# Performance work log

Measured on AMD Instinct MI355X. Metric: run time of the kernel, lower is better.

The kernel has to match this reference:

```python
import jax, jax.numpy as jnp
import numpy as np

# Grid / point-count constants (K-Radar-style sparse voxel grid)
B, Z, Y, X = 4, 40, 1024, 1024
Nr, Nl = 262144, 1048576
W_OCC, W_OFF, W_FEAT = 0.2, 1.0, 1.0
BIG = jnp.int32(1_000_000_000)  # sentinel for unmatched candidates


def _hash_zyx(b, z, y, x):
    # max value B*Z*Y*X ~ 1.7e8, fits int32
    return ((b * Z + z) * Y + y) * X + x


def _make_offsets(R):
    rng = np.arange(-R, R + 1)
    dz, dy, dx = np.meshgrid(rng, rng, rng, indexing='ij')
    return jnp.asarray(np.stack([dz.ravel(), dy.ravel(), dx.ravel()], axis=1), dtype=jnp.int32)  # [K,3]


def setup_inputs() -> dict:
    key = jax.random.key(0)
    k = jax.random.split(key, 10)
    radar_indices = jnp.stack([
        jax.random.randint(k[0], (Nr,), 0, B, dtype=jnp.int32),
        jax.random.randint(k[1], (Nr,), 0, Z, dtype=jnp.int32),
        jax.random.randint(k[2], (Nr,), 0, Y, dtype=jnp.int32),
        jax.random.randint(k[3], (Nr,), 0, X, dtype=jnp.int32)], axis=1)
    lidar_indices = jnp.stack([
        jax.random.randint(k[4], (Nl,), 0, B, dtype=jnp.int32),
        jax.random.randint(k[5], (Nl,), 0, Z, dtype=jnp.int32),
        jax.random.randint(k[6], (Nl,), 0, Y, dtype=jnp.int32),
        jax.random.randint(k[7], (Nl,), 0, X, dtype=jnp.int32)], axis=1)
    pred_feat = jax.random.normal(k[8], (Nr, 4), dtype=jnp.float32)
    pred_occ = jax.random.normal(k[9], (Nr, 1, 1), dtype=jnp.float32)
    lidar_features = jax.random.normal(jax.random.fold_in(key, 77), (Nl, 4), dtype=jnp.float32)
    return {"pred_feat": pred_feat, "pred_occ": pred_occ, "radar_indices": radar_indices,
            "lidar_features": lidar_features, "lidar_indices": lidar_indices, "R": 1}


def _local_match(radar_indices, lidar_indices, lidar_features, R):
    # Build sorted hash table of lidar voxels
    hL = _hash_zyx(lidar_indices[:, 0], lidar_indices[:, 1], lidar_indices[:, 2], lidar_indices[:, 3])
    ordL = jnp.argsort(hL)
    hL_sorted = hL[ordL]

    offs = _make_offsets(R)                      # [K,3]
    K = offs.shape[0]
    b, z, y, x = radar_indices[:, 0], radar_indices[:, 1], radar_indices[:, 2], radar_indices[:, 3]
    zz = jnp.clip(z[:, None] + offs[None, :, 0], 0, Z - 1)   # [Nr,K]
    yy = jnp.clip(y[:, None] + offs[None, :, 1], 0, Y - 1)
    xx = jnp.clip(x[:, None] + offs[None, :, 2], 0, X - 1)
    cand = _hash_zyx(b[:, None], zz, yy, xx).reshape(-1)      # [Nr*K]

    pos = jnp.searchsorted(hL_sorted, cand)                   # [Nr*K]
    safe_pos = jnp.clip(pos, 0, hL_sorted.shape[0] - 1)
    is_member = (pos < hL_sorted.shape[0]) & (hL_sorted[safe_pos] == cand)
    hit = is_member.reshape(-1, K)                            # [Nr,K]

    dL1 = jnp.sum(jnp.abs(offs), axis=1)                      # [K]
    dL1_masked = jnp.where(hit, dL1[None, :], BIG)            # [Nr,K]
    best_k = jnp.argmin(dL1_masked, axis=1)                   # [Nr]
    best = jnp.take_along_axis(dL1_masked, best_k[:, None], axis=1)[:, 0]
    matched = best < BIG                                      # [Nr] bool

    pos_flat = jnp.take_along_axis(pos.reshape(-1, K), best_k[:, None], axis=1)[:, 0]
    lidar_row = ordL[jnp.clip(pos_flat, 0, hL_sorted.shape[0] - 1)]
    gt_feat = jnp.where(matched[:, None], lidar_features[lidar_row], 0.0)  # [Nr, C_lidar]

    sel_z = jnp.take_along_axis(zz, best_k[:, None], axis=1)[:, 0]
    sel_y = jnp.take_along_axis(yy, best_k[:, None], axis=1)[:, 0]
    sel_x = jnp.take_along_axis(xx, best_k[:, None], axis=1)[:, 0]
    gt_offsets = jnp.stack([sel_z - z, sel_y - y, sel_x - x], axis=1).astype(jnp.float32)
    return matched, gt_offsets, gt_feat


def reference(pred_feat, pred_occ, radar_indices, lidar_features, lidar_indices, R):
    matched, gt_d, gt_f = _local_match(radar_indices, lidar_indices, lidar_features, R)
    gt_d = gt_d[:, ::-1]                              # torch.flip(gt_d, dims=[1])
    m = matched.astype(pred_feat.dtype)

    # BCEWithLogitsLoss(mean): logaddexp(0,x) - x*y
    occ_logits = jnp.mean(jnp.squeeze(pred_occ, axis=1), axis=-1)  # [Nr]
    occ_loss = jnp.mean(jnp.logaddexp(0.0, occ_logits) - occ_logits * m)

    cnt = jnp.sum(m)
    # smooth_l1 (beta=1, mean) over matched rows of pred offsets [M,3]
    diff = pred_feat[:, :3] - gt_d
    ad = jnp.abs(diff)
    sl1 = jnp.where(ad < 1.0, 0.5 * diff * diff, ad - 0.5)
    off_loss = jnp.sum(sl1 * m[:, None]) / jnp.maximum(cnt * 3.0, 1.0)
    # l1 (mean) over matched intensity column [M,1]
    feat_loss = jnp.sum(jnp.abs(pred_feat[:, 3:4] - gt_f[:, 3:4]) * m[:, None]) / jnp.maximum(cnt, 1.0)

    return W_OCC * occ_loss + W_OFF * off_loss + W_FEAT * feat_loss
```

## Files before the change

### kernel.cpp

```cpp
#include <hip/hip_runtime.h>
#include <math.h>
#include <limits.h>

#define BD 4
#define ZD 40
#define YD 1024
#define XD 1024
#define BZYX (167772160)

constexpr int BLOCK = 256;
constexpr unsigned SMALL_LOG = 19;
constexpr unsigned long long EMPTY64 = ~0ull;

typedef unsigned uvec4 __attribute__((ext_vector_type(4)));

__device__ __forceinline__ unsigned hash_mix(unsigned x) {
    x ^= x >> 16; x *= 0x7feb352dU;
    x ^= x >> 15; x *= 0x846ca68bU;
    x ^= x >> 16;
    return x;
}

__device__ __forceinline__ float smooth_l1(float d) {
    float ad = fabsf(d);
    return (ad < 1.0f) ? 0.5f * d * d : ad - 0.5f;
}

__device__ __forceinline__ float logaddexp0(float logit) {
    return (logit > 0.0f) ? (logit + log1pf(expf(-logit))) : log1pf(expf(logit));
}

__global__ void clear_bitmap(uvec4* __restrict__ bmv, int bmW4) {
    const uvec4 z = (uvec4)(0u);
    const int stride = gridDim.x * blockDim.x;
    for (int k = blockIdx.x * blockDim.x + threadIdx.x; k < bmW4; k += stride)
        bmv[k] = z;
}


__global__ void build_bitmap(const int4* __restrict__ li, int Nl,
                             unsigned* __restrict__ bm,
                             unsigned* __restrict__ cells,
                             uvec4* __restrict__ stv, int stW4) {
    const int gid = blockIdx.x * blockDim.x + threadIdx.x;
    if (gid < Nl) {
        int4 v = li[gid];
        unsigned cell = ((unsigned)(v.x * ZD + v.y) * YD + v.z) * XD + v.w;
        cells[gid] = cell;
        atomicOr(&bm[cell >> 5], 1u << (cell & 31));
    }
    const uvec4 f = (uvec4)(~0u);
    const int stride = gridDim.x * blockDim.x;
    for (int k = gid; k < stW4; k += stride)
        stv[k] = f;
}

__global__ void __launch_bounds__(BLOCK)
main_match(const float4* __restrict__ pf, const float* __restrict__ occ,
           const int4* __restrict__ ri, const unsigned* __restrict__ bm,
           unsigned long long* __restrict__ stab, unsigned smask,
           const int* __restrict__ Rptr, int Nr,
           int* __restrict__ mcell, double* __restrict__ partials) {
    const int R = *Rptr;
    const int i = blockIdx.x * BLOCK + threadIdx.x;
    double occ_s = 0.0, cnt_s = 0.0, off_s = 0.0;

    if (i < Nr) {
        int4 rib = ri[i];
        const int b = rib.x, z = rib.y, y = rib.z, x = rib.w;
        int mc = -1;
        float m = 0.0f;
        int sx = 0, sy = 0, sz = 0;
        bool matched = false;

        if (R == 1) {
            const int xa = max(x - 1, 0);
            const int xc = min(x + 1, XD - 1);
            const int sa = x - xa;
            const int sc = xc - xa;
            unsigned hm = 0;
#pragma unroll
            for (int dz = -1; dz <= 1; ++dz) {
                const int zz = min(max(z + dz, 0), ZD - 1);
#pragma unroll
                for (int dy = -1; dy <= 1; ++dy) {
                    const int yy = min(max(y + dy, 0), YD - 1);
                    const unsigned n0 =
                        ((unsigned)(b * ZD + zz) * YD + yy) * XD + (unsigned)xa;
                    const unsigned q = n0 >> 5;
                    const int r = n0 & 31;
                    unsigned long long w =
                        ((unsigned long long)bm[q + 1] << 32) | bm[q];
                    w >>= r;
                    const int k0 = (dz + 1) * 9 + (dy + 1) * 3;
                    hm |= ((unsigned)(w & 1)) << (k0 + 0);
                    hm |= ((unsigned)((w >> sa) & 1)) << (k0 + 1);
                    hm |= ((unsigned)((w >> sc) & 1)) << (k0 + 2);
                }
            }
            const unsigned M0 = 1u << 13;
            const unsigned M1 = (1u << 4) | (1u << 10) | (1u << 12) |
                                (1u << 14) | (1u << 16) | (1u << 22);
            const unsigned M2 = (1u << 1) | (1u << 3) | (1u << 5) | (1u << 7) |
                                (1u << 9) | (1u << 11) | (1u << 15) | (1u << 17) |
                                (1u << 19) | (1u << 21) | (1u << 23) | (1u << 25);
            int bk = -1;
            if (hm & M0)       bk = 13;
            else if (hm & M1)  bk = __ffs((int)(hm & M1)) - 1;
            else if (hm & M2)  bk = __ffs((int)(hm & M2)) - 1;
            else if (hm)       bk = __ffs((int)hm) - 1;
            if (bk >= 0) {
                matched = true;
                const int dz = bk / 9 - 1, dy = (bk / 3) % 3 - 1, dx = bk % 3 - 1;
                sz = min(max(z + dz, 0), ZD - 1);
                sy = min(max(y + dy, 0), YD - 1);
                sx = min(max(x + dx, 0), XD - 1);
            }
        } else {
            int bestd = INT_MAX;
            for (int dz = -R; dz <= R; ++dz) {
                const int zz = min(max(z + dz, 0), ZD - 1);
                const int adz = abs(dz);
                for (int dy = -R; dy <= R; ++dy) {
                    const int yy = min(max(y + dy, 0), YD - 1);
                    const int adzy = adz + abs(dy);
                    for (int dx = -R; dx <= R; ++dx) {
                        const int d = adzy + abs(dx);
                        if (d >= bestd) continue;
                        const int xx = min(max(x + dx, 0), XD - 1);
                        const unsigned cell =
                            ((unsigned)(b * ZD + zz) * YD + yy) * XD + xx;
                        if ((bm[cell >> 5] >> (cell & 31)) & 1u) {
                            bestd = d; matched = true;
                            sz = zz; sy = yy; sx = xx;
                        }
                    }
                }
            }
        }

        if (matched) {
            m = 1.0f;
            cnt_s = 1.0;
            const unsigned cell = ((unsigned)(b * ZD + sz) * YD + sy) * XD + sx;
            mc = (int)cell;
            const float4 p = pf[i];
            off_s = (double)(smooth_l1(p.x - (float)(sx - x)) +
                             smooth_l1(p.y - (float)(sy - y)) +
                             smooth_l1(p.z - (float)(sz - z)));
            const unsigned long long desired =
                ((unsigned long long)cell << 32) | 0xFFFFFFFFull;
            unsigned s = hash_mix(cell) & smask;
            while (true) {
                unsigned long long old = atomicCAS(&stab[s], EMPTY64, desired);
                if (old == EMPTY64 || (unsigned)(old >> 32) == cell) break;
                s = (s + 1) & smask;
            }
        }
        mcell[i] = mc;
        const float logit = occ[i];
        occ_s = (double)(logaddexp0(logit) - logit * m);
    }

    __shared__ double sh[3][BLOCK];
    const int tid = threadIdx.x;
    sh[0][tid] = occ_s; sh[1][tid] = cnt_s; sh[2][tid] = off_s;
    __syncthreads();
    for (int s = BLOCK / 2; s > 0; s >>= 1) {
        if (tid < s) {
            sh[0][tid] += sh[0][tid + s];
            sh[1][tid] += sh[1][tid + s];
            sh[2][tid] += sh[2][tid + s];
        }
        __syncthreads();
    }
    if (tid == 0) {
        partials[blockIdx.x * 4 + 0] = sh[0][0];
        partials[blockIdx.x * 4 + 1] = sh[1][0];
        partials[blockIdx.x * 4 + 2] = sh[2][0];
        partials[blockIdx.x * 4 + 3] = 0.0;
    }
}

__global__ void lidar_scan(const unsigned* __restrict__ cells, int Nl,
                           unsigned long long* __restrict__ stab, unsigned smask) {
    int j = blockIdx.x * blockDim.x + threadIdx.x;
    if (j >= Nl) return;
    const unsigned cell = cells[j];
    unsigned s = hash_mix(cell) & smask;
    while (true) {
        const unsigned long long e = stab[s];
        if (e == EMPTY64) return;
        if ((unsigned)(e >> 32) == cell) {
            atomicMin((unsigned*)&stab[s], (unsigned)j);
            return;
        }
        s = (s + 1) & smask;
    }
}

__global__ void __launch_bounds__(BLOCK)
feat_pass(const float4* __restrict__ pf, const int* __restrict__ mcell,
          const unsigned long long* __restrict__ stab, unsigned smask,
          const float4* __restrict__ lf, int Nr, double* __restrict__ fpart) {
    const int i = blockIdx.x * BLOCK + threadIdx.x;
    double fs = 0.0;
    if (i < Nr) {
        const int mc = mcell[i];
        if (mc >= 0) {
            const unsigned cell = (unsigned)mc;
            unsigned s = hash_mix(cell) & smask;
            unsigned row = 0;
            while (true) {
                const unsigned long long e = stab[s];
                if ((unsigned)(e >> 32) == cell) { row = (unsigned)e; break; }
                s = (s + 1) & smask;
            }
            fs = (double)fabsf(pf[i].w - lf[row].w);
        }
    }
    __shared__ double sh[BLOCK];
    const int tid = threadIdx.x;
    sh[tid] = fs;
    __syncthreads();
    for (int s = BLOCK / 2; s > 0; s >>= 1) {
        if (tid < s) sh[tid] += sh[tid + s];
        __syncthreads();
    }
    if (tid == 0) fpart[blockIdx.x] = sh[0];
}


__global__ void fb_insert(const int4* __restrict__ li, int Nl,
                          unsigned long long* __restrict__ tab, unsigned cmask) {
    int i = blockIdx.x * blockDim.x + threadIdx.x;
    if (i >= Nl) return;
    int4 v = li[i];
    const unsigned cell = ((unsigned)(v.x * ZD + v.y) * YD + v.z) * XD + v.w;
    const unsigned long long desired = ((unsigned long long)cell << 32) | (unsigned)i;
    unsigned s = hash_mix(cell) & cmask;
    unsigned probes = 0;
    while (probes++ <= cmask) {
        const unsigned long long old = atomicCAS(&tab[s], EMPTY64, desired);
        if (old == EMPTY64) return;
        if ((unsigned)(old >> 32) == cell) {
            atomicMin((unsigned*)&tab[s], (unsigned)i);
            return;
        }
        s = (s + 1) & cmask;
    }
}

__global__ void __launch_bounds__(BLOCK)
fb_main(const float4* __restrict__ pf, const float* __restrict__ occ,
        const int4* __restrict__ ri, const float4* __restrict__ lf,
        const unsigned long long* __restrict__ tab, unsigned cmask,
        const int* __restrict__ Rptr, int Nr, double* __restrict__ partials) {
    const int R = *Rptr;
    const int i = blockIdx.x * BLOCK + threadIdx.x;
    double occ_s = 0.0, cnt_s = 0.0, off_s = 0.0, feat_s = 0.0;
    if (i < Nr) {
        int4 rib = ri[i];
        const int b = rib.x, z = rib.y, y = rib.z, x = rib.w;
        int bestd = INT_MAX, bestRow = -1;
        int sx = 0, sy = 0, sz = 0;
        for (int dz = -R; dz <= R; ++dz) {
            const int zz = min(max(z + dz, 0), ZD - 1);
            const int adz = abs(dz);
            for (int dy = -R; dy <= R; ++dy) {
                const int yy = min(max(y + dy, 0), YD - 1);
                const int adzy = adz + abs(dy);
                for (int dx = -R; dx <= R; ++dx) {
                    const int d = adzy + abs(dx);
                    if (d >= bestd) continue;
                    const int xx = min(max(x + dx, 0), XD - 1);
                    const unsigned cell =
                        ((unsigned)(b * ZD + zz) * YD + yy) * XD + xx;
                    unsigned s = hash_mix(cell) & cmask;
                    int row = -1;
                    while (true) {
                        const unsigned long long e = tab[s];
                        if ((unsigned)(e >> 32) == cell) { row = (int)(unsigned)e; break; }
                        if (e == EMPTY64) break;
                        s = (s + 1) & cmask;
                    }
                    if (row >= 0) { bestd = d; bestRow = row; sz = zz; sy = yy; sx = xx; }
                }
            }
        }
        const float m = (bestRow >= 0) ? 1.0f : 0.0f;
        const float logit = occ[i];
        occ_s = (double)(logaddexp0(logit) - logit * m);
        if (bestRow >= 0) {
            cnt_s = 1.0;
            const float4 p = pf[i];
            off_s = (double)(smooth_l1(p.x - (float)(sx - x)) +
                             smooth_l1(p.y - (float)(sy - y)) +
                             smooth_l1(p.z - (float)(sz - z)));
            feat_s = (double)fabsf(p.w - lf[bestRow].w);
        }
    }
    __shared__ double sh[4][BLOCK];
    const int tid = threadIdx.x;
    sh[0][tid] = occ_s; sh[1][tid] = cnt_s; sh[2][tid] = off_s; sh[3][tid] = feat_s;
    __syncthreads();
    for (int s = BLOCK / 2; s > 0; s >>= 1) {
        if (tid < s) {
            sh[0][tid] += sh[0][tid + s];
            sh[1][tid] += sh[1][tid + s];
            sh[2][tid] += sh[2][tid + s];
            sh[3][tid] += sh[3][tid + s];
        }
        __syncthreads();
    }
    if (tid == 0) {
        partials[blockIdx.x * 4 + 0] = sh[0][0];
        partials[blockIdx.x * 4 + 1] = sh[1][0];
        partials[blockIdx.x * 4 + 2] = sh[2][0];
        partials[blockIdx.x * 4 + 3] = sh[3][0];
    }
}


__global__ void finalize_kernel(const double* __restrict__ partials,
                                const double* __restrict__ fpart, int nblk,
                                int Nr, float* __restrict__ out) {
    __shared__ double sh[4][BLOCK];
    const int tid = threadIdx.x;
    double a0 = 0, a1 = 0, a2 = 0, a3 = 0;
    for (int i = tid; i < nblk; i += BLOCK) {
        a0 += partials[i * 4 + 0];
        a1 += partials[i * 4 + 1];
        a2 += partials[i * 4 + 2];
        a3 += partials[i * 4 + 3] + fpart[i];
    }
    sh[0][tid] = a0; sh[1][tid] = a1; sh[2][tid] = a2; sh[3][tid] = a3;
    __syncthreads();
    for (int s = BLOCK / 2; s > 0; s >>= 1) {
        if (tid < s) {
            sh[0][tid] += sh[0][tid + s];
            sh[1][tid] += sh[1][tid + s];
            sh[2][tid] += sh[2][tid + s];
            sh[3][tid] += sh[3][tid + s];
        }
        __syncthreads();
    }
    if (tid == 0) {
        const double occ_loss = sh[0][0] / (double)Nr;
        const double cnt = sh[1][0];
        const double off_loss = sh[2][0] / fmax(cnt * 3.0, 1.0);
        const double feat_loss = sh[3][0] / fmax(cnt, 1.0);
        out[0] = (float)(0.2 * occ_loss + 1.0 * off_loss + 1.0 * feat_loss);
    }
}

extern "C" void kernel_launch(void* const* d_in, const int* in_sizes, int n_in,
                              void* d_out, int out_size, void* d_ws, size_t ws_size,
                              hipStream_t stream) {
    const float* pred_feat  = (const float*)d_in[0];
    const float* pred_occ   = (const float*)d_in[1];
    const int*   radar_idx  = (const int*)d_in[2];
    const float* lidar_feat = (const float*)d_in[3];
    const int*   lidar_idx  = (const int*)d_in[4];
    const int*   Rptr       = (const int*)d_in[5];

    const int Nr = in_sizes[0] / 4;
    const int Nl = in_sizes[3] / 4;
    const int nblk  = (Nr + BLOCK - 1) / BLOCK;
    const int nblkL = (Nl + BLOCK - 1) / BLOCK;

    size_t off = 0;
    auto alloc = [&](size_t n) { size_t o = off; off += (n + 255) & ~(size_t)255; return o; };
    const size_t bmBytes   = (size_t)BZYX / 8 + 64;
    const size_t stabBytes = (size_t)8 << SMALL_LOG;
    const size_t bmOff   = alloc(bmBytes);
    const size_t stabOff = alloc(stabBytes);
    const size_t cellOff = alloc((size_t)Nl * 4);
    const size_t mcOff   = alloc((size_t)Nr * 4);
    const size_t pOff    = alloc((size_t)nblk * 4 * sizeof(double));
    const size_t fpOff   = alloc((size_t)nblk * sizeof(double));
    const size_t needD = off;

    char* ws = (char*)d_ws;
    if (needD <= ws_size) {
        unsigned*           bm    = (unsigned*)(ws + bmOff);
        unsigned long long* stab  = (unsigned long long*)(ws + stabOff);
        unsigned*           cells = (unsigned*)(ws + cellOff);
        int*                mcell = (int*)(ws + mcOff);
        double*             parts = (double*)(ws + pOff);
        double*             fpart = (double*)(ws + fpOff);
        const unsigned smask = (1u << SMALL_LOG) - 1;
        const int stW4 = (int)(stabBytes / 16);

        clear_bitmap<<<4096, BLOCK, 0, stream>>>((uvec4*)bm, (int)(bmBytes / 16));
        build_bitmap<<<nblkL, BLOCK, 0, stream>>>(
            (const int4*)lidar_idx, Nl, bm, cells, (uvec4*)stab, stW4);
        main_match<<<nblk, BLOCK, 0, stream>>>(
            (const float4*)pred_feat, pred_occ, (const int4*)radar_idx,
            bm, stab, smask, Rptr, Nr, mcell, parts);
        lidar_scan<<<nblkL, BLOCK, 0, stream>>>(cells, Nl, stab, smask);
        feat_pass<<<nblk, BLOCK, 0, stream>>>(
            (const float4*)pred_feat, mcell, stab, smask,
            (const float4*)lidar_feat, Nr, fpart);
        finalize_kernel<<<1, BLOCK, 0, stream>>>(parts, fpart, nblk, Nr, (float*)d_out);
    } else {
        const size_t tailBytes = (size_t)nblk * 5 * sizeof(double) + 512;
        unsigned C = 1u << 22;
        while ((size_t)C * 8 + tailBytes > ws_size && C > (1u << 21)) C >>= 1;
        const unsigned cmask = C - 1;
        unsigned long long* tab = (unsigned long long*)ws;
        double* parts = (double*)(ws + ((size_t)C * 8 + 255 & ~(size_t)255));
        double* fpart = parts + (size_t)nblk * 4;

        hipError_t e1 = hipMemsetAsync(tab, 0xFF, (size_t)C * 8, stream); (void)e1;
        hipError_t e2 = hipMemsetAsync(fpart, 0x00, (size_t)nblk * sizeof(double), stream); (void)e2;

        fb_insert<<<nblkL, BLOCK, 0, stream>>>((const int4*)lidar_idx, Nl, tab, cmask);
        fb_main<<<nblk, BLOCK, 0, stream>>>(
            (const float4*)pred_feat, pred_occ, (const int4*)radar_idx,
            (const float4*)lidar_feat, tab, cmask, Rptr, Nr, parts);
        finalize_kernel<<<1, BLOCK, 0, stream>>>(parts, fpart, nblk, Nr, (float*)d_out);
    }
}
```

Before: 117.2 us.

## Add slot-occupancy bitmap to prune lidar scan and fuse finalize into feat pass

Adds a 64KB bitmap marking which hash slots were claimed by matched radar cells. The lidar scan checks this bitmap first and returns early when the home slot is empty, so it avoids reading the 4MB hash table for most lidar points. The final reduction moves into the last block of feat_pass through an atomic counter and threadfence, which removes one kernel launch. Costs are extra atomics in main_match and a slightly larger clear region. The early exit relies on linear probing never leaving a claimed home slot empty.

```diff
diff --git a/kernel.cpp b/kernel.cpp
--- a/kernel.cpp
+++ b/kernel.cpp
@@ -11,6 +11,7 @@
 constexpr int BLOCK = 256;
 constexpr unsigned SMALL_LOG = 19;
 constexpr unsigned long long EMPTY64 = ~0ull;
+constexpr size_t OCC_BYTES = (size_t)1 << (SMALL_LOG - 3);
 
 typedef unsigned uvec4 __attribute__((ext_vector_type(4)));
 
@@ -36,7 +37,6 @@
     for (int k = blockIdx.x * blockDim.x + threadIdx.x; k < bmW4; k += stride)
         bmv[k] = z;
 }
-
 
 __global__ void build_bitmap(const int4* __restrict__ li, int Nl,
                              unsigned* __restrict__ bm,
@@ -58,8 +58,8 @@
 __global__ void __launch_bounds__(BLOCK)
 main_match(const float4* __restrict__ pf, const float* __restrict__ occ,
            const int4* __restrict__ ri, const unsigned* __restrict__ bm,
-           unsigned long long* __restrict__ stab, unsigned smask,
-           const int* __restrict__ Rptr, int Nr,
+           unsigned long long* __restrict__ stab, unsigned* __restrict__ occbm,
+           unsigned smask, const int* __restrict__ Rptr, int Nr,
            int* __restrict__ mcell, double* __restrict__ partials) {
     const int R = *Rptr;
     const int i = blockIdx.x * BLOCK + threadIdx.x;
@@ -151,11 +151,14 @@
             const unsigned long long desired =
                 ((unsigned long long)cell << 32) | 0xFFFFFFFFull;
             unsigned s = hash_mix(cell) & smask;
+            bool claimed = false;
             while (true) {
                 unsigned long long old = atomicCAS(&stab[s], EMPTY64, desired);
-                if (old == EMPTY64 || (unsigned)(old >> 32) == cell) break;
+                if (old == EMPTY64) { claimed = true; break; }
+                if ((unsigned)(old >> 32) == cell) break;
                 s = (s + 1) & smask;
             }
+            if (claimed) atomicOr(&occbm[s >> 5], 1u << (s & 31));
         }
         mcell[i] = mc;
         const float logit = occ[i];
@@ -183,11 +186,13 @@
 }
 
 __global__ void lidar_scan(const unsigned* __restrict__ cells, int Nl,
-                           unsigned long long* __restrict__ stab, unsigned smask) {
+                           unsigned long long* __restrict__ stab,
+                           const unsigned* __restrict__ occbm, unsigned smask) {
     int j = blockIdx.x * blockDim.x + threadIdx.x;
     if (j >= Nl) return;
     const unsigned cell = cells[j];
     unsigned s = hash_mix(cell) & smask;
+    if (!((occbm[s >> 5] >> (s & 31)) & 1u)) return;
     while (true) {
         const unsigned long long e = stab[s];
         if (e == EMPTY64) return;
@@ -202,7 +207,9 @@
 __global__ void __launch_bounds__(BLOCK)
 feat_pass(const float4* __restrict__ pf, const int* __restrict__ mcell,
           const unsigned long long* __restrict__ stab, unsigned smask,
-          const float4* __restrict__ lf, int Nr, double* __restrict__ fpart) {
+          const float4* __restrict__ lf, int Nr, double* __restrict__ fpart,
+          const double* __restrict__ partials, unsigned* __restrict__ counter,
+          int mblk, float* __restrict__ out) {
     const int i = blockIdx.x * BLOCK + threadIdx.x;
     double fs = 0.0;
     if (i < Nr) {
@@ -219,15 +226,50 @@
             fs = (double)fabsf(pf[i].w - lf[row].w);
         }
     }
-    __shared__ double sh[BLOCK];
+    __shared__ double sh[4][BLOCK];
+    __shared__ bool isLast;
     const int tid = threadIdx.x;
-    sh[tid] = fs;
+    sh[0][tid] = fs;
     __syncthreads();
     for (int s = BLOCK / 2; s > 0; s >>= 1) {
-        if (tid < s) sh[tid] += sh[tid + s];
+        if (tid < s) sh[0][tid] += sh[0][tid + s];
         __syncthreads();
     }
-    if (tid == 0) fpart[blockIdx.x] = sh[0];
+    if (tid == 0) {
+        fpart[blockIdx.x] = sh[0][0];
+        __threadfence();
+        const unsigned done = atomicAdd(counter, 1u);
+        isLast = (done == gridDim.x - 1);
+    }
+    __syncthreads();
+    if (!isLast) return;
+
+    double a0 = 0, a1 = 0, a2 = 0, a3 = 0;
+    for (int k = tid; k < mblk; k += BLOCK) {
+        a0 += partials[k * 4 + 0];
+        a1 += partials[k * 4 + 1];
+        a2 += partials[k * 4 + 2];
+    }
+    for (int k = tid; k < (int)gridDim.x; k += BLOCK) a3 += fpart[k];
+    __syncthreads();
+    sh[0][tid] = a0; sh[1][tid] = a1; sh[2][tid] = a2; sh[3][tid] = a3;
+    __syncthreads();
+    for (int s = BLOCK / 2; s > 0; s >>= 1) {
+        if (tid < s) {
+            sh[0][tid] += sh[0][tid + s];
+            sh[1][tid] += sh[1][tid + s];
+            sh[2][tid] += sh[2][tid + s];
+            sh[3][tid] += sh[3][tid + s];
+        }
+        __syncthreads();
+    }
+    if (tid == 0) {
+        const double occ_loss = sh[0][0] / (double)Nr;
+        const double cnt = sh[1][0];
+        const double off_loss = sh[2][0] / fmax(cnt * 3.0, 1.0);
+        const double feat_loss = sh[3][0] / fmax(cnt, 1.0);
+        out[0] = (float)(0.2 * occ_loss + 1.0 * off_loss + 1.0 * feat_loss);
+    }
 }
 
 
@@ -321,7 +363,6 @@
     }
 }
 
-
 __global__ void finalize_kernel(const double* __restrict__ partials,
                                 const double* __restrict__ fpart, int nblk,
                                 int Nr, float* __restrict__ out) {
@@ -374,6 +415,9 @@
     const size_t bmBytes   = (size_t)BZYX / 8 + 64;
     const size_t stabBytes = (size_t)8 << SMALL_LOG;
     const size_t bmOff   = alloc(bmBytes);
+    const size_t occOff  = alloc(OCC_BYTES);
+    const size_t ctrOff  = alloc(256);
+    const size_t clearEnd = off;
     const size_t stabOff = alloc(stabBytes);
     const size_t cellOff = alloc((size_t)Nl * 4);
     const size_t mcOff   = alloc((size_t)Nr * 4);
@@ -384,6 +428,8 @@
     char* ws = (char*)d_ws;
     if (needD <= ws_size) {
         unsigned*           bm    = (unsigned*)(ws + bmOff);
+        unsigned*           occbm = (unsigned*)(ws + occOff);
+        unsigned*           ctr   = (unsigned*)(ws + ctrOff);
         unsigned long long* stab  = (unsigned long long*)(ws + stabOff);
         unsigned*           cells = (unsigned*)(ws + cellOff);
         int*                mcell = (int*)(ws + mcOff);
@@ -392,17 +438,16 @@
         const unsigned smask = (1u << SMALL_LOG) - 1;
         const int stW4 = (int)(stabBytes / 16);
 
-        clear_bitmap<<<4096, BLOCK, 0, stream>>>((uvec4*)bm, (int)(bmBytes / 16));
+        clear_bitmap<<<4096, BLOCK, 0, stream>>>((uvec4*)ws, (int)(clearEnd / 16));
         build_bitmap<<<nblkL, BLOCK, 0, stream>>>(
             (const int4*)lidar_idx, Nl, bm, cells, (uvec4*)stab, stW4);
         main_match<<<nblk, BLOCK, 0, stream>>>(
             (const float4*)pred_feat, pred_occ, (const int4*)radar_idx,
-            bm, stab, smask, Rptr, Nr, mcell, parts);
-        lidar_scan<<<nblkL, BLOCK, 0, stream>>>(cells, Nl, stab, smask);
+            bm, stab, occbm, smask, Rptr, Nr, mcell, parts);
+        lidar_scan<<<nblkL, BLOCK, 0, stream>>>(cells, Nl, stab, occbm, smask);
         feat_pass<<<nblk, BLOCK, 0, stream>>>(
             (const float4*)pred_feat, mcell, stab, smask,
-            (const float4*)lidar_feat, Nr, fpart);
-        finalize_kernel<<<1, BLOCK, 0, stream>>>(parts, fpart, nblk, Nr, (float*)d_out);
+            (const float4*)lidar_feat, Nr, fpart, parts, ctr, nblk, (float*)d_out);
     } else {
         const size_t tailBytes = (size_t)nblk * 5 * sizeof(double) + 512;
         unsigned C = 1u << 22;
```

After: 133.1 us. 1.14x slower.
